# Performance work log

Hardware: AMD Instinct MI355X
Metric: run time of the kernel (lower is better)

The kernel has to match this reference:

```python
import jax, jax.numpy as jnp
import numpy as np


def setup_inputs() -> dict:
    key = jax.random.key(0)
    k1, k2, k3 = jax.random.split(key, 3)
    B, K, C, H, W = 8, 8, 256, 64, 64
    return {
        "IR_features": jax.random.normal(k1, (B, K, C, H, W), dtype=jnp.float32),
        "CR_features": jax.random.normal(k2, (B, K, C, H, W), dtype=jnp.float32),
        "CT_feature": jax.random.normal(k3, (B, C, H, W), dtype=jnp.float32),
    }


def reference(IR_features, CR_features, CT_feature):
    # sim: [B, K, C, 1, 1] = <CT, CR>_{HW} / ||CR||_{HW}
    dot = jnp.sum(CT_feature[:, None] * CR_features, axis=(3, 4), keepdims=True)
    norm = jnp.sqrt(jnp.sum(CR_features ** 2, axis=(3, 4), keepdims=True))
    sim = dot / norm
    weights = jax.nn.softmax(sim * 2.0, axis=1)  # softmax over K styles
    # style feature: weighted sum over K -> [B, C, H, W]
    style_feature = jnp.sum(IR_features * weights, axis=1)
    return style_feature
```

## Files before the change

### kernel.cpp

```cpp
#include <hip/hip_runtime.h>
#include <math.h>

#define B_DIM 8
#define K_DIM 8
#define C_DIM 256
#define HW4   1024

__global__ __launch_bounds__(256, 4)
void dfs_sim(const float4* __restrict__ CR,
             const float4* __restrict__ CT,
             float* __restrict__ sims)
{
    const int bid = blockIdx.x;
    const int k   = bid & 7;
    const int bc  = bid >> 3;
    const int b   = bc >> 8;
    const int c   = bc & 255;
    const int t   = threadIdx.x;

    const float4* __restrict__ ctp = CT + (size_t)bc * HW4;
    const float4* __restrict__ crp = CR + (size_t)((b * K_DIM + k) * C_DIM + c) * HW4;

    float4 a[4], r[4];
#pragma unroll
    for (int i = 0; i < 4; ++i) {
        a[i] = ctp[t + i * 256];
        r[i] = crp[t + i * 256];
    }
    float d = 0.f, s = 0.f;
#pragma unroll
    for (int i = 0; i < 4; ++i) {
        d = fmaf(a[i].x, r[i].x, d); d = fmaf(a[i].y, r[i].y, d);
        d = fmaf(a[i].z, r[i].z, d); d = fmaf(a[i].w, r[i].w, d);
        s = fmaf(r[i].x, r[i].x, s); s = fmaf(r[i].y, r[i].y, s);
        s = fmaf(r[i].z, r[i].z, s); s = fmaf(r[i].w, r[i].w, s);
    }

#pragma unroll
    for (int off = 32; off >= 1; off >>= 1) {
        d += __shfl_xor(d, off, 64);
        s += __shfl_xor(s, off, 64);
    }
    __shared__ float rd[4], rs[4];
    const int wave = t >> 6, lane = t & 63;
    if (lane == 0) { rd[wave] = d; rs[wave] = s; }
    __syncthreads();
    if (t == 0) {
        const float dd = rd[0] + rd[1] + rd[2] + rd[3];
        const float ss = rs[0] + rs[1] + rs[2] + rs[3];
        sims[bid] = 2.0f * dd / sqrtf(ss);
    }
}

__global__ __launch_bounds__(256, 4)
void dfs_mix(const float4* __restrict__ IR,
             const float* __restrict__ sims,
             float4* __restrict__ out)
{
    const int bc = blockIdx.x;
    const int b  = bc >> 8;
    const int c  = bc & 255;
    const int t  = threadIdx.x;

    float si[K_DIM];
#pragma unroll
    for (int j = 0; j < K_DIM; ++j) si[j] = sims[bc * K_DIM + j];
    float m = si[0];
#pragma unroll
    for (int j = 1; j < K_DIM; ++j) m = fmaxf(m, si[j]);
    float w[K_DIM];
    float sum = 0.f;
#pragma unroll
    for (int j = 0; j < K_DIM; ++j) { w[j] = expf(si[j] - m); sum += w[j]; }
    const float inv = 1.0f / sum;
#pragma unroll
    for (int j = 0; j < K_DIM; ++j) w[j] *= inv;

    const size_t plane0  = (size_t)(b * K_DIM * C_DIM + c) * HW4;
    const size_t kstride = (size_t)C_DIM * HW4;
    const size_t obase   = (size_t)bc * HW4;

#pragma unroll
    for (int i = 0; i < 4; ++i) {
        const int off = t + i * 256;
        float4 v[K_DIM];
#pragma unroll
        for (int j = 0; j < K_DIM; ++j) v[j] = IR[plane0 + j * kstride + off];
        float4 acc = make_float4(0.f, 0.f, 0.f, 0.f);
#pragma unroll
        for (int j = 0; j < K_DIM; ++j) {
            acc.x = fmaf(w[j], v[j].x, acc.x);
            acc.y = fmaf(w[j], v[j].y, acc.y);
            acc.z = fmaf(w[j], v[j].z, acc.z);
            acc.w = fmaf(w[j], v[j].w, acc.w);
        }
        out[obase + off] = acc;
    }
}

extern "C" void kernel_launch(void* const* d_in, const int* in_sizes, int n_in,
                              void* d_out, int out_size, void* d_ws, size_t ws_size,
                              hipStream_t stream) {
    const float4* IR = (const float4*)d_in[0];
    const float4* CR = (const float4*)d_in[1];
    const float4* CT = (const float4*)d_in[2];
    float4* out      = (float4*)d_out;
    float* sims      = (float*)d_ws;

    dfs_sim<<<B_DIM * C_DIM * K_DIM, 256, 0, stream>>>(CR, CT, sims);
    dfs_mix<<<B_DIM * C_DIM, 256, 0, stream>>>(IR, sims, out);
}
```

Measured before the change: 530.4 us.

## Fuse similarity and mixing kernels into one per-(b,c) block with nontemporal loads

Merges the similarity kernel and the mixing kernel into a single kernel with one block per (b,c). Each wave computes dot products and norms for two of the K styles, and softmax weights are exchanged through shared memory. This removes a launch, the workspace round trip, and the eightfold re-read of CT across blocks. CR and IR are read with nontemporal loads to reduce cache pollution. Only 2048 blocks remain, so each block now streams a much larger share of data serially, which may reduce latency hiding.

```diff
diff --git a/kernel.cpp b/kernel.cpp
--- a/kernel.cpp
+++ b/kernel.cpp
@@ -6,65 +6,85 @@
 #define C_DIM 256
 #define HW4   1024
 
+typedef float v4f __attribute__((ext_vector_type(4)));
+
+__device__ __forceinline__ float4 nt_load4(const float4* p) {
+    v4f v = __builtin_nontemporal_load(reinterpret_cast<const v4f*>(p));
+    return make_float4(v.x, v.y, v.z, v.w);
+}
+
 __global__ __launch_bounds__(256, 4)
-void dfs_sim(const float4* __restrict__ CR,
-             const float4* __restrict__ CT,
-             float* __restrict__ sims)
+void dfs_fused2(const float4* __restrict__ IR,
+                const float4* __restrict__ CR,
+                const float4* __restrict__ CT,
+                float4* __restrict__ out)
 {
-    const int bid = blockIdx.x;
-    const int k   = bid & 7;
-    const int bc  = bid >> 3;
-    const int b   = bc >> 8;
-    const int c   = bc & 255;
-    const int t   = threadIdx.x;
+    const int bc   = blockIdx.x;
+    const int b    = bc >> 8;
+    const int c    = bc & 255;
+    const int t    = threadIdx.x;
+    const int wave = t >> 6;
+    const int lane = t & 63;
 
-    const float4* __restrict__ ctp = CT + (size_t)bc * HW4;
-    const float4* __restrict__ crp = CR + (size_t)((b * K_DIM + k) * C_DIM + c) * HW4;
+    const size_t ct_base = (size_t)bc * HW4;
 
-    float4 a[4], r[4];
+    const int k0 = wave;
+    const int k1 = wave + 4;
+    const size_t cr0b = (size_t)((b * K_DIM + k0) * C_DIM + c) * HW4;
+    const size_t cr1b = (size_t)((b * K_DIM + k1) * C_DIM + c) * HW4;
+
+    float d0 = 0.f, s0 = 0.f, d1 = 0.f, s1 = 0.f;
 #pragma unroll
     for (int i = 0; i < 4; ++i) {
-        a[i] = ctp[t + i * 256];
-        r[i] = crp[t + i * 256];
-    }
-    float d = 0.f, s = 0.f;
+        float4 a[4], r0[4], r1[4];
 #pragma unroll
-    for (int i = 0; i < 4; ++i) {
-        d = fmaf(a[i].x, r[i].x, d); d = fmaf(a[i].y, r[i].y, d);
-        d = fmaf(a[i].z, r[i].z, d); d = fmaf(a[i].w, r[i].w, d);
-        s = fmaf(r[i].x, r[i].x, s); s = fmaf(r[i].y, r[i].y, s);
-        s = fmaf(r[i].z, r[i].z, s); s = fmaf(r[i].w, r[i].w, s);
+        for (int j = 0; j < 4; ++j) {
+            const int off = lane + j * 64 + i * 256;
+            a[j] = CT[ct_base + off];
+        }
+#pragma unroll
+        for (int j = 0; j < 4; ++j) {
+            const int off = lane + j * 64 + i * 256;
+            r0[j] = nt_load4(&CR[cr0b + off]);
+        }
+#pragma unroll
+        for (int j = 0; j < 4; ++j) {
+            const int off = lane + j * 64 + i * 256;
+            r1[j] = nt_load4(&CR[cr1b + off]);
+        }
+#pragma unroll
+        for (int j = 0; j < 4; ++j) {
+            d0 = fmaf(a[j].x, r0[j].x, d0); d0 = fmaf(a[j].y, r0[j].y, d0);
+            d0 = fmaf(a[j].z, r0[j].z, d0); d0 = fmaf(a[j].w, r0[j].w, d0);
+            s0 = fmaf(r0[j].x, r0[j].x, s0); s0 = fmaf(r0[j].y, r0[j].y, s0);
+            s0 = fmaf(r0[j].z, r0[j].z, s0); s0 = fmaf(r0[j].w, r0[j].w, s0);
+            d1 = fmaf(a[j].x, r1[j].x, d1); d1 = fmaf(a[j].y, r1[j].y, d1);
+            d1 = fmaf(a[j].z, r1[j].z, d1); d1 = fmaf(a[j].w, r1[j].w, d1);
+            s1 = fmaf(r1[j].x, r1[j].x, s1); s1 = fmaf(r1[j].y, r1[j].y, s1);
+            s1 = fmaf(r1[j].w, r1[j].w, s1); s1 = fmaf(r1[j].z, r1[j].z, s1);
+        }
     }
 
 #pragma unroll
     for (int off = 32; off >= 1; off >>= 1) {
-        d += __shfl_xor(d, off, 64);
-        s += __shfl_xor(s, off, 64);
+        d0 += __shfl_xor(d0, off, 64);
+        s0 += __shfl_xor(s0, off, 64);
+        d1 += __shfl_xor(d1, off, 64);
+        s1 += __shfl_xor(s1, off, 64);
     }
-    __shared__ float rd[4], rs[4];
-    const int wave = t >> 6, lane = t & 63;
-    if (lane == 0) { rd[wave] = d; rs[wave] = s; }
+
+    __shared__ float sd[K_DIM], ss[K_DIM], simv[K_DIM];
+    if (lane == 0) {
+        sd[k0] = d0; ss[k0] = s0;
+        sd[k1] = d1; ss[k1] = s1;
+    }
     __syncthreads();
-    if (t == 0) {
-        const float dd = rd[0] + rd[1] + rd[2] + rd[3];
-        const float ss = rs[0] + rs[1] + rs[2] + rs[3];
-        sims[bid] = 2.0f * dd / sqrtf(ss);
-    }
-}
-
-__global__ __launch_bounds__(256, 4)
-void dfs_mix(const float4* __restrict__ IR,
-             const float* __restrict__ sims,
-             float4* __restrict__ out)
-{
-    const int bc = blockIdx.x;
-    const int b  = bc >> 8;
-    const int c  = bc & 255;
-    const int t  = threadIdx.x;
+    if (t < K_DIM) simv[t] = 2.0f * sd[t] / sqrtf(ss[t]);
+    __syncthreads();
 
     float si[K_DIM];
 #pragma unroll
-    for (int j = 0; j < K_DIM; ++j) si[j] = sims[bc * K_DIM + j];
+    for (int j = 0; j < K_DIM; ++j) si[j] = simv[j];
     float m = si[0];
 #pragma unroll
     for (int j = 1; j < K_DIM; ++j) m = fmaxf(m, si[j]);
@@ -78,14 +98,14 @@
 
     const size_t plane0  = (size_t)(b * K_DIM * C_DIM + c) * HW4;
     const size_t kstride = (size_t)C_DIM * HW4;
-    const size_t obase   = (size_t)bc * HW4;
 
 #pragma unroll
     for (int i = 0; i < 4; ++i) {
         const int off = t + i * 256;
         float4 v[K_DIM];
 #pragma unroll
-        for (int j = 0; j < K_DIM; ++j) v[j] = IR[plane0 + j * kstride + off];
+        for (int j = 0; j < K_DIM; ++j)
+            v[j] = nt_load4(&IR[plane0 + j * kstride + off]);
         float4 acc = make_float4(0.f, 0.f, 0.f, 0.f);
 #pragma unroll
         for (int j = 0; j < K_DIM; ++j) {
@@ -94,7 +114,7 @@
             acc.z = fmaf(w[j], v[j].z, acc.z);
             acc.w = fmaf(w[j], v[j].w, acc.w);
         }
-        out[obase + off] = acc;
+        out[ct_base + off] = acc;
     }
 }
 
@@ -105,8 +125,6 @@
     const float4* CR = (const float4*)d_in[1];
     const float4* CT = (const float4*)d_in[2];
     float4* out      = (float4*)d_out;
-    float* sims      = (float*)d_ws;
 
-    dfs_sim<<<B_DIM * C_DIM * K_DIM, 256, 0, stream>>>(CR, CT, sims);
-    dfs_mix<<<B_DIM * C_DIM, 256, 0, stream>>>(IR, sims, out);
+    dfs_fused2<<<B_DIM * C_DIM, 256, 0, stream>>>(IR, CR, CT, out);
 }
```

Measured after the change: 520.6 us. About the same (-1.9%).
